# Kernel tuning notes

Measured on AMD Instinct MI355X. Metric: run time of the kernel, lower is better.

## Reference

```python
import jax, jax.numpy as jnp
import numpy as np
import math

EMBED_DIM = 768
NUM_HEADS = 12
MLP_HIDDEN = int(EMBED_DIM * 2.0)
LN_EPS = 1e-6


def _complex_linear(r, i, wr, wi, br, bi):
    # (r + i*j) @ (wr + wi*j)^T + (br + bi*j)
    out_r = r @ wr.T - i @ wi.T + br
    out_i = r @ wi.T + i @ wr.T + bi
    return out_r, out_i


def _complex_layernorm(r, i, gamma, beta):
    # magnitude-based LN over feature dim; gamma/beta: [F, 2]
    mag = jnp.sqrt(r * r + i * i + LN_EPS)           # [..., F]
    mean = mag.mean(axis=-1, keepdims=True)
    var = ((mag - mean) ** 2).mean(axis=-1, keepdims=True)  # unbiased=False
    norm_mag = (mag - mean) / jnp.sqrt(var + LN_EPS)
    scale = norm_mag / (mag + LN_EPS)
    r_n = r * scale
    i_n = i * scale
    return gamma[..., 0] * r_n + beta[..., 0], gamma[..., 1] * i_n + beta[..., 1]


def setup_inputs() -> dict:
    key = jax.random.key(0)
    ks = jax.random.split(key, 12)
    B, N, E, H = 2, 2048, EMBED_DIM, MLP_HIDDEN
    std_qkv = math.sqrt(2.0 / (E + 3 * E))
    std_proj = math.sqrt(2.0 / (E + E))
    std_fc1 = math.sqrt(2.0 / (E + H))
    std_fc2 = math.sqrt(2.0 / (H + E))
    inp = {
        "x": jax.random.normal(ks[0], (B, N, 2 * E), dtype=jnp.float32),
        "norm1_gamma": 1.0 + 0.1 * jax.random.normal(ks[1], (E, 2), dtype=jnp.float32),
        "norm1_beta": 0.1 * jax.random.normal(ks[2], (E, 2), dtype=jnp.float32),
        "qkv_wr": std_qkv * jax.random.normal(ks[3], (3 * E, E), dtype=jnp.float32),
        "qkv_wi": std_qkv * jax.random.normal(ks[4], (3 * E, E), dtype=jnp.float32),
        "qkv_br": jnp.zeros((3 * E,), dtype=jnp.float32),
        "qkv_bi": jnp.zeros((3 * E,), dtype=jnp.float32),
        "proj_wr": std_proj * jax.random.normal(ks[5], (E, E), dtype=jnp.float32),
        "proj_wi": std_proj * jax.random.normal(ks[6], (E, E), dtype=jnp.float32),
        "proj_br": jnp.zeros((E,), dtype=jnp.float32),
        "proj_bi": jnp.zeros((E,), dtype=jnp.float32),
        "norm2_gamma": 1.0 + 0.1 * jax.random.normal(ks[7], (E, 2), dtype=jnp.float32),
        "norm2_beta": 0.1 * jax.random.normal(ks[8], (E, 2), dtype=jnp.float32),
        "fc1_wr": std_fc1 * jax.random.normal(ks[9], (H, E), dtype=jnp.float32),
        "fc1_wi": std_fc1 * jax.random.normal(ks[10], (H, E), dtype=jnp.float32),
        "fc1_br": jnp.zeros((H,), dtype=jnp.float32),
        "fc1_bi": jnp.zeros((H,), dtype=jnp.float32),
        "fc2_wr": std_fc2 * jax.random.normal(ks[11], (E, H), dtype=jnp.float32),
        "fc2_wi": std_fc2 * jax.random.normal(jax.random.fold_in(key, 99), (E, H), dtype=jnp.float32),
        "fc2_br": jnp.zeros((E,), dtype=jnp.float32),
        "fc2_bi": jnp.zeros((E,), dtype=jnp.float32),
    }
    return inp


def reference(x, norm1_gamma, norm1_beta, qkv_wr, qkv_wi, qkv_br, qkv_bi,
              proj_wr, proj_wi, proj_br, proj_bi, norm2_gamma, norm2_beta,
              fc1_wr, fc1_wi, fc1_br, fc1_bi, fc2_wr, fc2_wi, fc2_br, fc2_bi):
    B, N, _ = x.shape
    E, nH = EMBED_DIM, NUM_HEADS
    hd = E // nH
    xc = x.reshape(B, N, E, 2)
    xr, xi = xc[..., 0], xc[..., 1]

    # --- attention branch ---
    nr, ni = _complex_layernorm(xr, xi, norm1_gamma, norm1_beta)
    qkv_r, qkv_i = _complex_linear(nr, ni, qkv_wr, qkv_wi, qkv_br, qkv_bi)  # [B,N,3E]
    # split to [3, B, nH, N, hd]
    def split_heads(t):
        return t.reshape(B, N, 3, nH, hd).transpose(2, 0, 3, 1, 4)
    qkv_r = split_heads(qkv_r)
    qkv_i = split_heads(qkv_i)
    qr, kr, vr = qkv_r[0], qkv_r[1], qkv_r[2]
    qi, ki, vi = qkv_i[0], qkv_i[1], qkv_i[2]

    # complex attention scores: q * conj-free formulation per source
    attn_real = jnp.einsum('bhqd,bhkd->bhqk', qr, kr) + jnp.einsum('bhqd,bhkd->bhqk', qi, ki)
    attn_imag = jnp.einsum('bhqd,bhkd->bhqk', qr, ki) - jnp.einsum('bhqd,bhkd->bhqk', qi, kr)
    attn_mag = jnp.sqrt(attn_real ** 2 + attn_imag ** 2 + 1e-8) / math.sqrt(hd)
    attn_w = jax.nn.softmax(attn_mag, axis=-1)
    out_r = jnp.einsum('bhqk,bhkd->bhqd', attn_w, vr)
    out_i = jnp.einsum('bhqk,bhkd->bhqd', attn_w, vi)
    # [B,nH,N,hd] -> [B,N,E]
    out_r = out_r.transpose(0, 2, 1, 3).reshape(B, N, E)
    out_i = out_i.transpose(0, 2, 1, 3).reshape(B, N, E)
    pr, pi = _complex_linear(out_r, out_i, proj_wr, proj_wi, proj_br, proj_bi)
    xr = xr + pr
    xi = xi + pi

    # --- MLP branch ---
    nr2, ni2 = _complex_layernorm(xr, xi, norm2_gamma, norm2_beta)
    h_r, h_i = _complex_linear(nr2, ni2, fc1_wr, fc1_wi, fc1_br, fc1_bi)
    h_r = jax.nn.gelu(h_r, approximate=False)
    h_i = jax.nn.gelu(h_i, approximate=False)
    m_r, m_i = _complex_linear(h_r, h_i, fc2_wr, fc2_wi, fc2_br, fc2_bi)
    xr = xr + m_r
    xi = xi + m_i

    return jnp.stack([xr, xi], axis=-1).reshape(B, N, 2 * E)
```

## Files before the change

### kernel.cpp

```cpp
#include <hip/hip_runtime.h>
#include <cmath>

typedef __bf16 bf16;
typedef __bf16 bf16x8 __attribute__((ext_vector_type(8)));
typedef __bf16 bf16x4 __attribute__((ext_vector_type(4)));
typedef float  f32x4  __attribute__((ext_vector_type(4)));
typedef unsigned int u32x4 __attribute__((ext_vector_type(4)));

#define MFMA16(a, b, c) __builtin_amdgcn_mfma_f32_16x16x32_bf16((a), (b), (c), 0, 0, 0)
#define LOG2E 1.44269504088896f

static __device__ __forceinline__ void gl_lds16(const void* g, void* l) {
    __builtin_amdgcn_global_load_lds((const __attribute__((address_space(1))) void*)g,
                                     (__attribute__((address_space(3))) void*)l, 16, 0, 0);
}

static __device__ __forceinline__ bf16x8 bneg8(bf16x8 x) {
    u32x4 u = __builtin_bit_cast(u32x4, x);
    u = u ^ 0x80008000u;
    return __builtin_bit_cast(bf16x8, u);
}

static __device__ __forceinline__ f32x4 zero4() {
    return f32x4{0.0f, 0.0f, 0.0f, 0.0f};
}

__global__ void fill_kernel(float* p, float v, int n) {
    for (int i = blockIdx.x * blockDim.x + threadIdx.x; i < n; i += gridDim.x * blockDim.x)
        p[i] = v;
}

struct Cvt8 {
    const float* s[8];
    bf16* d[8];
    int boff[9];
    int cvtBlocks;
};
__global__ __launch_bounds__(256) void prep_kernel(
    Cvt8 c, const float* __restrict__ x,
    const float* __restrict__ gamma, const float* __restrict__ beta,
    bf16* __restrict__ nr, bf16* __restrict__ ni) {
    const int t = threadIdx.x;
    if ((int)blockIdx.x < c.cvtBlocks) {
        int blk = blockIdx.x;
        int seg = 0;
#pragma unroll
        for (int k = 0; k < 7; ++k)
            if (blk >= c.boff[k + 1]) seg = k + 1;
        const int local = blk - c.boff[seg];
        const int i = local * 1024 + t * 4;
        const float4 v = *(const float4*)(c.s[seg] + i);
        bf16x4 o;
        o[0] = (bf16)v.x; o[1] = (bf16)v.y; o[2] = (bf16)v.z; o[3] = (bf16)v.w;
        *(bf16x4*)(c.d[seg] + i) = o;
        return;
    }
    __shared__ float red[4];
    const size_t base = (size_t)(blockIdx.x - c.cvtBlocks) * 768;
    float r[3], im[3], mg[3];
#pragma unroll
    for (int j = 0; j < 3; ++j) {
        const int f = t + j * 256;
        const float2 v = ((const float2*)x)[base + f];
        r[j] = v.x;
        im[j] = v.y;
        mg[j] = __builtin_amdgcn_sqrtf(r[j] * r[j] + im[j] * im[j] + 1e-6f);
    }
    float s = mg[0] + mg[1] + mg[2];
#pragma unroll
    for (int m = 32; m >= 1; m >>= 1) s += __shfl_xor(s, m);
    if ((t & 63) == 0) red[t >> 6] = s;
    __syncthreads();
    const float mean = (red[0] + red[1] + red[2] + red[3]) * (1.0f / 768.0f);
    __syncthreads();
    float v2 = 0.0f;
#pragma unroll
    for (int j = 0; j < 3; ++j) {
        const float d = mg[j] - mean;
        v2 += d * d;
    }
#pragma unroll
    for (int m = 32; m >= 1; m >>= 1) v2 += __shfl_xor(v2, m);
    if ((t & 63) == 0) red[t >> 6] = v2;
    __syncthreads();
    const float var = (red[0] + red[1] + red[2] + red[3]) * (1.0f / 768.0f);
    const float rstd = rsqrtf(var + 1e-6f);
#pragma unroll
    for (int j = 0; j < 3; ++j) {
        const int f = t + j * 256;
        const float sc = (mg[j] - mean) * rstd / (mg[j] + 1e-6f);
        nr[base + f] = (bf16)(gamma[2 * f] * (r[j] * sc) + beta[2 * f]);
        ni[base + f] = (bf16)(gamma[2 * f + 1] * (im[j] * sc) + beta[2 * f + 1]);
    }
}

__global__ __launch_bounds__(256) void cln2_kernel(
    const bf16* __restrict__ xa, const bf16* __restrict__ xb,
    const float* __restrict__ gamma, const float* __restrict__ beta,
    bf16* __restrict__ nr, bf16* __restrict__ ni) {
    __shared__ float red[4];
    const int t = threadIdx.x;
    const size_t base = (size_t)blockIdx.x * 768;

    float r[3], im[3], mg[3];
#pragma unroll
    for (int j = 0; j < 3; ++j) {
        const int f = t + j * 256;
        r[j] = (float)xa[base + f];
        im[j] = (float)xb[base + f];
        mg[j] = __builtin_amdgcn_sqrtf(r[j] * r[j] + im[j] * im[j] + 1e-6f);
    }
    float s = mg[0] + mg[1] + mg[2];
#pragma unroll
    for (int m = 32; m >= 1; m >>= 1) s += __shfl_xor(s, m);
    if ((t & 63) == 0) red[t >> 6] = s;
    __syncthreads();
    const float mean = (red[0] + red[1] + red[2] + red[3]) * (1.0f / 768.0f);
    __syncthreads();

    float v2 = 0.0f;
#pragma unroll
    for (int j = 0; j < 3; ++j) {
        const float d = mg[j] - mean;
        v2 += d * d;
    }
#pragma unroll
    for (int m = 32; m >= 1; m >>= 1) v2 += __shfl_xor(v2, m);
    if ((t & 63) == 0) red[t >> 6] = v2;
    __syncthreads();
    const float var = (red[0] + red[1] + red[2] + red[3]) * (1.0f / 768.0f);
    const float rstd = rsqrtf(var + 1e-6f);

#pragma unroll
    for (int j = 0; j < 3; ++j) {
        const int f = t + j * 256;
        const float sc = (mg[j] - mean) * rstd / (mg[j] + 1e-6f);
        nr[base + f] = (bf16)(gamma[2 * f] * (r[j] * sc) + beta[2 * f]);
        ni[base + f] = (bf16)(gamma[2 * f + 1] * (im[j] * sc) + beta[2 * f + 1]);
    }
}

template <int BM, int BN, int MODE, int OCC, bool SWZC>
__global__ __launch_bounds__(256, OCC) void cgemm_kernel(
    const bf16* __restrict__ Ar, const bf16* __restrict__ Ai,
    const bf16* __restrict__ Wr, const bf16* __restrict__ Wi,
    const float* __restrict__ br, const float* __restrict__ bi,
    const void* __restrict__ resr, const void* __restrict__ resi,
    float* __restrict__ outFr, float* __restrict__ outFi,
    bf16* __restrict__ outBr, bf16* __restrict__ outBi,
    int N, int K) {
    constexpr int MR = BM / 32;
    constexpr int NR = BN / 32;
    constexpr int ASEG = BM / 8;
    constexpr int NSEG = (BM + BN) / 8;
    constexpr int SPW = NSEG / 4;

    __shared__ __align__(16) bf16 sA[2][BM][64];
    __shared__ __align__(16) bf16 sB[2][BN][64];

    const int tid = threadIdx.x;
    const int wave = tid >> 6, lane = tid & 63;
    const int lg = lane >> 4, lr = lane & 15;

    const int bid = blockIdx.y * gridDim.x + blockIdx.x;
    const int xcd = bid & 7;
    const int i = bid >> 3;
    int rowb, colb;
    if (SWZC) {
        const int cpx = gridDim.y >> 3;
        colb = xcd * cpx + (i % cpx);
        rowb = i / cpx;
    } else {
        const int rpx = gridDim.x >> 3;
        rowb = xcd * rpx + (i % rpx);
        colb = i / rpx;
    }
    const int row0 = rowb * BM, col0 = colb * BN;

    const int wm = (wave >> 1) * (BM / 2), wn = (wave & 1) * (BN / 2);

    const int srow = lane >> 3;
    const int schunk = (lane & 7) ^ srow;
    const int spl = schunk >> 2;
    const int sc8 = (schunk & 3) * 8;

    auto issue = [&](int buf, int kt) {
#pragma unroll
        for (int s = 0; s < SPW; ++s) {
            const int id = wave * SPW + s;
            if (id < ASEG) {
                const int row = id * 8 + srow;
                gl_lds16((spl ? Ai : Ar) + (size_t)(row0 + row) * K + kt + sc8,
                         &sA[buf][id * 8][0]);
            } else {
                const int row = (id - ASEG) * 8 + srow;
                gl_lds16((spl ? Wi : Wr) + (size_t)(col0 + row) * K + kt + sc8,
                         &sB[buf][(id - ASEG) * 8][0]);
            }
        }
    };

    f32x4 accr[MR][NR], acci[MR][NR];
#pragma unroll
    for (int a = 0; a < MR; ++a)
#pragma unroll
        for (int b2 = 0; b2 < NR; ++b2) {
            accr[a][b2] = zero4();
            acci[a][b2] = zero4();
        }

    issue(0, 0);

    const int KT = K / 32;
    for (int kt = 0; kt < KT; ++kt) {
        const int buf = kt & 1;
        if (kt + 1 < KT) {
            issue(buf ^ 1, (kt + 1) * 32);
            __builtin_amdgcn_sched_barrier(0);
            if constexpr (SPW == 8)
                asm volatile("s_waitcnt vmcnt(8)" ::: "memory");
            else if constexpr (SPW == 6)
                asm volatile("s_waitcnt vmcnt(6)" ::: "memory");
            else
                asm volatile("s_waitcnt vmcnt(0)" ::: "memory");
        } else {
            asm volatile("s_waitcnt vmcnt(0)" ::: "memory");
        }
        __builtin_amdgcn_sched_barrier(0);
        __builtin_amdgcn_s_barrier();
        __builtin_amdgcn_sched_barrier(0);

        bf16x8 ar[MR], ai[MR], an[MR];
#pragma unroll
        for (int mt = 0; mt < MR; ++mt) {
            const int rr = wm + mt * 16 + lr;
            const int slr = lg ^ (rr & 7);
            const int sli = (4 + lg) ^ (rr & 7);
            ar[mt] = *(const bf16x8*)(&sA[buf][rr][slr * 8]);
            ai[mt] = *(const bf16x8*)(&sA[buf][rr][sli * 8]);
            an[mt] = bneg8(ai[mt]);
        }
        __builtin_amdgcn_s_setprio(1);
#pragma unroll
        for (int nt = 0; nt < NR; ++nt) {
            const int rr = wn + nt * 16 + lr;
            const int slr = lg ^ (rr & 7);
            const int sli = (4 + lg) ^ (rr & 7);
            const bf16x8 br8 = *(const bf16x8*)(&sB[buf][rr][slr * 8]);
            const bf16x8 bi8 = *(const bf16x8*)(&sB[buf][rr][sli * 8]);
#pragma unroll
            for (int mt = 0; mt < MR; ++mt) {
                accr[mt][nt] = MFMA16(ar[mt], br8, accr[mt][nt]);
                accr[mt][nt] = MFMA16(an[mt], bi8, accr[mt][nt]);
                acci[mt][nt] = MFMA16(ar[mt], bi8, acci[mt][nt]);
                acci[mt][nt] = MFMA16(ai[mt], br8, acci[mt][nt]);
            }
        }
        __builtin_amdgcn_s_setprio(0);

        if (kt + 1 < KT) {
            __builtin_amdgcn_sched_barrier(0);
            __builtin_amdgcn_s_barrier();
            __builtin_amdgcn_sched_barrier(0);
        }
    }

#pragma unroll
    for (int nt = 0; nt < NR; ++nt) {
        const int col = col0 + wn + nt * 16 + lr;
        const float bre = br[col], bie = bi[col];
#pragma unroll
        for (int mt = 0; mt < MR; ++mt) {
#pragma unroll
            for (int j = 0; j < 4; ++j) {
                const int row = row0 + wm + mt * 16 + lg * 4 + j;
                float vr = accr[mt][nt][j] + bre;
                float vi = acci[mt][nt][j] + bie;
                const size_t o = (size_t)row * N + col;
                if (MODE == 1) {
                    const float2 rv = ((const float2*)resr)[(size_t)row * 768 + col];
                    outBr[o] = (bf16)(rv.x + vr);
                    outBi[o] = (bf16)(rv.y + vi);
                } else if (MODE == 2) {
                    const float t2r = fmaf(vr * vr, 0.044715f, 1.0f);
                    const float er = __builtin_amdgcn_exp2f(vr * t2r * 2.3022082f);
                    vr = vr - vr * __builtin_amdgcn_rcpf(er + 1.0f);
                    const float t2i = fmaf(vi * vi, 0.044715f, 1.0f);
                    const float ei = __builtin_amdgcn_exp2f(vi * t2i * 2.3022082f);
                    vi = vi - vi * __builtin_amdgcn_rcpf(ei + 1.0f);
                    outBr[o] = (bf16)vr;
                    outBi[o] = (bf16)vi;
                } else {
                    const size_t ro = (size_t)row * 768 + col;
                    outFr[(size_t)row * 1536 + 2 * col] =
                        (float)((const bf16*)resr)[ro] + vr;
                    outFr[(size_t)row * 1536 + 2 * col + 1] =
                        (float)((const bf16*)resi)[ro] + vi;
                }
            }
        }
    }
}

__global__ __launch_bounds__(256, 3) void qkvt_kernel(
    const bf16* __restrict__ nr, const bf16* __restrict__ ni,
    const bf16* __restrict__ wqr, const bf16* __restrict__ wqi,
    const float* __restrict__ qbr, const float* __restrict__ qbi,
    bf16* __restrict__ qkr, bf16* __restrict__ qki,
    bf16* __restrict__ vtr, bf16* __restrict__ vti) {
    constexpr int BM = 64, BN = 128, K = 768;
    constexpr int MR = 2, NR = 4, ASEG = 8, SPW = 6;
    constexpr int HHE = 1536 * 768;

    __shared__ __align__(16) bf16 sA[2][BM][64];
    __shared__ __align__(16) bf16 sB[2][BN][64];

    const int tid = threadIdx.x;
    const int wave = tid >> 6, lane = tid & 63;
    const int lg = lane >> 4, lr = lane & 15;

    const bool isQK = (int)blockIdx.x < 768;
    const bf16 *Ar, *Ai, *Wr, *Wi;
    bf16 *outR, *outI;
    int N, row0, col0;
    if (isQK) {
        const int bid = blockIdx.x;
        const int xcd = bid & 7, i = bid >> 3;
        row0 = (xcd * 8 + (i & 7)) * BM;
        col0 = (i >> 3) * BN;
        Ar = nr; Ai = ni; Wr = wqr; Wi = wqi;
        outR = qkr; outI = qki; N = 1536;
    } else {
        const int bid = blockIdx.x - 768;
        const int xcd = bid & 7, i = bid >> 3;
        col0 = (xcd * 4 + (i & 3)) * BN;
        row0 = (i >> 2) * BM;
        Ar = wqr + HHE; Ai = wqi + HHE; Wr = nr; Wi = ni;
        outR = vtr; outI = vti; N = 4096;
    }

    const int wm = (wave >> 1) * (BM / 2), wn = (wave & 1) * (BN / 2);
    const int srow = lane >> 3;
    const int schunk = (lane & 7) ^ srow;
    const int spl = schunk >> 2;
    const int sc8 = (schunk & 3) * 8;

    auto issue = [&](int buf, int kt) {
#pragma unroll
        for (int s = 0; s < SPW; ++s) {
            const int id = wave * SPW + s;
            if (id < ASEG) {
                const int row = id * 8 + srow;
                gl_lds16((spl ? Ai : Ar) + (size_t)(row0 + row) * K + kt + sc8,
                         &sA[buf][id * 8][0]);
            } else {
                const int row = (id - ASEG) * 8 + srow;
                gl_lds16((spl ? Wi : Wr) + (size_t)(col0 + row) * K + kt + sc8,
                         &sB[buf][(id - ASEG) * 8][0]);
            }
        }
    };

    f32x4 accr[MR][NR], acci[MR][NR];
#pragma unroll
    for (int a = 0; a < MR; ++a)
#pragma unroll
        for (int b2 = 0; b2 < NR; ++b2) {
            accr[a][b2] = zero4();
            acci[a][b2] = zero4();
        }

    issue(0, 0);

    const int KT = K / 32;
    for (int kt = 0; kt < KT; ++kt) {
        const int buf = kt & 1;
        if (kt + 1 < KT) {
            issue(buf ^ 1, (kt + 1) * 32);
            __builtin_amdgcn_sched_barrier(0);
            asm volatile("s_waitcnt vmcnt(6)" ::: "memory");
        } else {
            asm volatile("s_waitcnt vmcnt(0)" ::: "memory");
        }
        __builtin_amdgcn_sched_barrier(0);
        __builtin_amdgcn_s_barrier();
        __builtin_amdgcn_sched_barrier(0);

        bf16x8 ar[MR], ai[MR], an[MR];
#pragma unroll
        for (int mt = 0; mt < MR; ++mt) {
            const int rr = wm + mt * 16 + lr;
            const int slr = lg ^ (rr & 7);
            const int sli = (4 + lg) ^ (rr & 7);
            ar[mt] = *(const bf16x8*)(&sA[buf][rr][slr * 8]);
            ai[mt] = *(const bf16x8*)(&sA[buf][rr][sli * 8]);
            an[mt] = bneg8(ai[mt]);
        }
        __builtin_amdgcn_s_setprio(1);
#pragma unroll
        for (int nt = 0; nt < NR; ++nt) {
            const int rr = wn + nt * 16 + lr;
            const int slr = lg ^ (rr & 7);
            const int sli = (4 + lg) ^ (rr & 7);
            const bf16x8 br8 = *(const bf16x8*)(&sB[buf][rr][slr * 8]);
            const bf16x8 bi8 = *(const bf16x8*)(&sB[buf][rr][sli * 8]);
#pragma unroll
            for (int mt = 0; mt < MR; ++mt) {
                accr[mt][nt] = MFMA16(ar[mt], br8, accr[mt][nt]);
                accr[mt][nt] = MFMA16(an[mt], bi8, accr[mt][nt]);
                acci[mt][nt] = MFMA16(ar[mt], bi8, acci[mt][nt]);
                acci[mt][nt] = MFMA16(ai[mt], br8, acci[mt][nt]);
            }
        }
        __builtin_amdgcn_s_setprio(0);

        if (kt + 1 < KT) {
            __builtin_amdgcn_sched_barrier(0);
            __builtin_amdgcn_s_barrier();
            __builtin_amdgcn_sched_barrier(0);
        }
    }

#pragma unroll
    for (int nt = 0; nt < NR; ++nt) {
        const int col = col0 + wn + nt * 16 + lr;
        const float bre = isQK ? qbr[col] : 0.0f;
        const float bie = isQK ? qbi[col] : 0.0f;
#pragma unroll
        for (int mt = 0; mt < MR; ++mt) {
#pragma unroll
            for (int j = 0; j < 4; ++j) {
                const int row = row0 + wm + mt * 16 + lg * 4 + j;
                float vr = accr[mt][nt][j];
                float vi = acci[mt][nt][j];
                if (isQK) {
                    vr += bre;
                    vi += bie;
                } else {
                    vr += qbr[1536 + row];
                    vi += qbi[1536 + row];
                }
                const size_t o = (size_t)row * N + col;
                outR[o] = (bf16)vr;
                outI[o] = (bf16)vi;
            }
        }
    }
}

__global__ __launch_bounds__(256, 3) void cattn_kernel(
    const bf16* __restrict__ qkr, const bf16* __restrict__ qki,
    const bf16* __restrict__ vtr, const bf16* __restrict__ vti,
    bf16* __restrict__ aor, bf16* __restrict__ aoi) {
    __shared__ __align__(16) bf16 sK[3][2][32][64];
    __shared__ __align__(16) bf16 sV[3][64][64];
    __shared__ __align__(16) bf16 sP[4][16][40];

    const int tid = threadIdx.x;
    const int w = tid >> 6, lane = tid & 63;
    const int lg = lane >> 4, lr = lane & 15;

    const int bid = blockIdx.x;
    const int xcd = bid & 7;
    const int i = bid >> 3;
    const int grp = xcd * 3 + (i >> 5);
    const int qb = i & 31;
    const int h = grp % 12, b = grp / 12;
    const int ld = 1536;

    const int s_krow = lane >> 3;
    const int s_kch8 = ((lane & 7) ^ s_krow) * 8;
    const int s_vlog = (lane & 7) ^ s_krow;
    const int s_vpl = s_vlog >> 2;
    const int s_vk8 = (s_vlog & 3) * 8;

    const bf16* kbase0 = qkr + (size_t)b * 2048 * ld + 768 + h * 64;
    const bf16* kbase1 = qki + (size_t)b * 2048 * ld + 768 + h * 64;
    const bf16* vbase = (s_vpl ? vti : vtr) + (size_t)(h * 64) * 4096 + b * 2048;

    const bf16* kp0 = kbase0 + (size_t)(w * 8 + s_krow) * ld + s_kch8;
    const bf16* kp1 = kbase1 + (size_t)(w * 8 + s_krow) * ld + s_kch8;
    const bf16* vp0 = vbase + (size_t)(w * 8 + s_krow) * 4096 + s_vk8;
    const bf16* vp1 = vbase + (size_t)((4 + w) * 8 + s_krow) * 4096 + s_vk8;

    auto stage = [&](int slot) {
        gl_lds16(kp0, &sK[slot][0][w * 8][0]);
        gl_lds16(kp1, &sK[slot][1][w * 8][0]);
        gl_lds16(vp0, &sV[slot][w * 8][0]);
        gl_lds16(vp1, &sV[slot][(4 + w) * 8][0]);
        kp0 += 32 * ld;
        kp1 += 32 * ld;
        vp0 += 32;
        vp1 += 32;
    };

    stage(0);

    const size_t qoff = (size_t)(b * 2048 + qb * 64 + w * 16 + lr) * ld + h * 64;
    bf16x8 aqr[2], aqi[2], aqin[2];
#pragma unroll
    for (int ks = 0; ks < 2; ++ks) {
        aqr[ks] = *(const bf16x8*)(qkr + qoff + ks * 32 + lg * 8);
        aqi[ks] = *(const bf16x8*)(qki + qoff + ks * 32 + lg * 8);
        aqin[ks] = bneg8(aqi[ks]);
    }

    f32x4 our[4], oui[4];
#pragma unroll
    for (int d = 0; d < 4; ++d) {
        our[d] = zero4();
        oui[d] = zero4();
    }
    const float C1 = 0.125f * LOG2E;
    float mrun = -1e30f;
    float lrun_p = 0.0f;
    float thr2 = -1.0f;
    float mC2 = 0.0f;

    int cur = 0;
    const int slr = lg ^ (lr & 7);
    const int sli = (4 + lg) ^ (lr & 7);

    for (int kt = 0; kt < 64; ++kt) {
        int nxt = cur + 1;
        if (nxt == 3) nxt = 0;
        if (kt < 63) {
            stage(nxt);
            __builtin_amdgcn_sched_barrier(0);
            asm volatile("s_waitcnt vmcnt(4)" ::: "memory");
        } else {
            asm volatile("s_waitcnt vmcnt(0)" ::: "memory");
        }
        __builtin_amdgcn_sched_barrier(0);
        __builtin_amdgcn_s_barrier();
        __builtin_amdgcn_sched_barrier(0);

        f32x4 str[2], sti[2];
        str[0] = zero4(); str[1] = zero4();
        sti[0] = zero4(); sti[1] = zero4();
        __builtin_amdgcn_s_setprio(1);
#pragma unroll
        for (int t = 0; t < 2; ++t) {
#pragma unroll
            for (int ks = 0; ks < 2; ++ks) {
                const int ch = ((ks << 2) | lg) ^ (lr & 7);
                const bf16x8 kr8 = *(const bf16x8*)(&sK[cur][0][t * 16 + lr][ch * 8]);
                const bf16x8 ki8 = *(const bf16x8*)(&sK[cur][1][t * 16 + lr][ch * 8]);
                str[t] = MFMA16(kr8, aqr[ks], str[t]);
                str[t] = MFMA16(ki8, aqi[ks], str[t]);
                sti[t] = MFMA16(ki8, aqr[ks], sti[t]);
                sti[t] = MFMA16(kr8, aqin[ks], sti[t]);
            }
        }
        __builtin_amdgcn_s_setprio(0);

        float v[8];
        float vmax = 0.0f;
#pragma unroll
        for (int t = 0; t < 2; ++t)
#pragma unroll
            for (int j = 0; j < 4; ++j) {
                const float sr = str[t][j], si = sti[t][j];
                const float vv = fmaf(sr, sr, fmaf(si, si, 1e-8f));
                v[t * 4 + j] = vv;
                vmax = fmaxf(vmax, vv);
            }

        if (!__all(vmax <= thr2)) {
            vmax = fmaxf(vmax, __shfl_xor(vmax, 16));
            vmax = fmaxf(vmax, __shfl_xor(vmax, 32));
            const float tm = __builtin_amdgcn_sqrtf(vmax) * 0.125f;
            const float mnew = fmaxf(mrun, tm);
            const float corr = __builtin_amdgcn_exp2f((mrun - mnew) * LOG2E);
            float cj[4];
#pragma unroll
            for (int j = 0; j < 4; ++j) cj[j] = __shfl(corr, lg * 4 + j);
#pragma unroll
            for (int d = 0; d < 4; ++d)
#pragma unroll
                for (int j = 0; j < 4; ++j) {
                    our[d][j] *= cj[j];
                    oui[d][j] *= cj[j];
                }
            lrun_p *= corr;
            mrun = mnew;
            const float m8 = mrun + 8.0f;
            thr2 = 64.0f * m8 * m8;
            mC2 = -mrun * LOG2E;
        }

        float p[8];
        float ls = 0.0f;
#pragma unroll
        for (int i2 = 0; i2 < 8; ++i2) {
            p[i2] = __builtin_amdgcn_exp2f(
                fmaf(__builtin_amdgcn_sqrtf(v[i2]), C1, mC2));
            ls += p[i2];
        }
        lrun_p += ls;

#pragma unroll
        for (int t = 0; t < 2; ++t) {
            bf16x4 pk;
#pragma unroll
            for (int j = 0; j < 4; ++j) pk[j] = (bf16)p[t * 4 + j];
            *(bf16x4*)(&sP[w][lr][t * 16 + lg * 4]) = pk;
        }
        const bf16x8 pf = *(const bf16x8*)(&sP[w][lr][lg * 8]);

        __builtin_amdgcn_s_setprio(1);
#pragma unroll
        for (int d = 0; d < 4; ++d) {
            const bf16x8 vr8 = *(const bf16x8*)(&sV[cur][d * 16 + lr][slr * 8]);
            const bf16x8 vi8 = *(const bf16x8*)(&sV[cur][d * 16 + lr][sli * 8]);
            our[d] = MFMA16(pf, vr8, our[d]);
            oui[d] = MFMA16(pf, vi8, oui[d]);
        }
        __builtin_amdgcn_s_setprio(0);

        cur = nxt;
    }

    float lsum = lrun_p;
    lsum += __shfl_xor(lsum, 16);
    lsum += __shfl_xor(lsum, 32);

    float linv[4];
#pragma unroll
    for (int j = 0; j < 4; ++j) {
        const float lj = __shfl(lsum, lg * 4 + j);
        linv[j] = __builtin_amdgcn_rcpf(lj);
    }
#pragma unroll
    for (int d = 0; d < 4; ++d)
#pragma unroll
        for (int j = 0; j < 4; ++j) {
            const int row = b * 2048 + qb * 64 + w * 16 + lg * 4 + j;
            const int col = h * 64 + d * 16 + lr;
            aor[(size_t)row * 768 + col] = (bf16)(our[d][j] * linv[j]);
            aoi[(size_t)row * 768 + col] = (bf16)(oui[d][j] * linv[j]);
        }
}

extern "C" void kernel_launch(void* const* d_in, const int* in_sizes, int n_in,
                              void* d_out, int out_size, void* d_ws, size_t ws_size,
                              hipStream_t stream) {
    const float* x      = (const float*)d_in[0];
    const float* n1g    = (const float*)d_in[1];
    const float* n1b    = (const float*)d_in[2];
    const float* qkvwr  = (const float*)d_in[3];
    const float* qkvwi  = (const float*)d_in[4];
    const float* qkvbr  = (const float*)d_in[5];
    const float* qkvbi  = (const float*)d_in[6];
    const float* projwr = (const float*)d_in[7];
    const float* projwi = (const float*)d_in[8];
    const float* projbr = (const float*)d_in[9];
    const float* projbi = (const float*)d_in[10];
    const float* n2g    = (const float*)d_in[11];
    const float* n2b    = (const float*)d_in[12];
    const float* fc1wr  = (const float*)d_in[13];
    const float* fc1wi  = (const float*)d_in[14];
    const float* fc1br  = (const float*)d_in[15];
    const float* fc1bi  = (const float*)d_in[16];
    const float* fc2wr  = (const float*)d_in[17];
    const float* fc2wi  = (const float*)d_in[18];
    const float* fc2br  = (const float*)d_in[19];
    const float* fc2bi  = (const float*)d_in[20];

    const int M = 4096, E = 768, E3 = 2304, HH = 1536;

    char* base = (char*)d_ws;
    size_t off = 0;
    auto alloc = [&](size_t bytes) -> void* {
        void* p = base + off;
        off += (bytes + 255) & ~(size_t)255;
        return p;
    };
    bf16* xr2  = (bf16*)alloc((size_t)M * E * 2);
    bf16* xi2  = (bf16*)alloc((size_t)M * E * 2);
    bf16* nr   = (bf16*)alloc((size_t)M * E * 2);
    bf16* ni   = (bf16*)alloc((size_t)M * E * 2);
    bf16* wqr  = (bf16*)alloc((size_t)E3 * E * 2);
    bf16* wqi  = (bf16*)alloc((size_t)E3 * E * 2);
    bf16* wpr  = (bf16*)alloc((size_t)E * E * 2);
    bf16* wpi  = (bf16*)alloc((size_t)E * E * 2);
    bf16* w1r  = (bf16*)alloc((size_t)HH * E * 2);
    bf16* w1i  = (bf16*)alloc((size_t)HH * E * 2);
    bf16* w2r  = (bf16*)alloc((size_t)E * HH * 2);
    bf16* w2i  = (bf16*)alloc((size_t)E * HH * 2);
    bf16* qkr  = (bf16*)alloc((size_t)M * HH * 2);
    bf16* qki  = (bf16*)alloc((size_t)M * HH * 2);
    bf16* vtr  = (bf16*)alloc((size_t)E * M * 2);
    bf16* vti  = (bf16*)alloc((size_t)E * M * 2);
    bf16* aor  = (bf16*)alloc((size_t)M * E * 2);
    bf16* aoi  = (bf16*)alloc((size_t)M * E * 2);
    bf16* hr   = (bf16*)alloc((size_t)M * HH * 2);
    bf16* hi   = (bf16*)alloc((size_t)M * HH * 2);

    if (off > ws_size) {
        fill_kernel<<<1024, 256, 0, stream>>>((float*)d_out, 1.0e9f, out_size);
        return;
    }

    Cvt8 c;
    c.s[0] = qkvwr; c.d[0] = wqr;
    c.s[1] = qkvwi; c.d[1] = wqi;
    c.s[2] = projwr; c.d[2] = wpr;
    c.s[3] = projwi; c.d[3] = wpi;
    c.s[4] = fc1wr; c.d[4] = w1r;
    c.s[5] = fc1wi; c.d[5] = w1i;
    c.s[6] = fc2wr; c.d[6] = w2r;
    c.s[7] = fc2wi; c.d[7] = w2i;
    const int nseg[8] = {E3 * E, E3 * E, E * E, E * E, HH * E, HH * E, E * HH, E * HH};
    int cum = 0;
    for (int k = 0; k < 8; ++k) {
        c.boff[k] = cum;
        cum += nseg[k] / 1024;
    }
    c.boff[8] = cum;
    c.cvtBlocks = cum;
    prep_kernel<<<cum + M, 256, 0, stream>>>(c, x, n1g, n1b, nr, ni);

    qkvt_kernel<<<1152, 256, 0, stream>>>(nr, ni, wqr, wqi, qkvbr, qkvbi,
                                          qkr, qki, vtr, vti);
    cattn_kernel<<<768, 256, 0, stream>>>(qkr, qki, vtr, vti, aor, aoi);
    cgemm_kernel<128, 64, 1, 3, false><<<dim3(32, 12), 256, 0, stream>>>(
        aor, aoi, wpr, wpi, projbr, projbi, x, nullptr, nullptr, nullptr,
        xr2, xi2, E, E);
    cln2_kernel<<<M, 256, 0, stream>>>(xr2, xi2, n2g, n2b, nr, ni);
    cgemm_kernel<64, 128, 2, 3, false><<<dim3(64, 12), 256, 0, stream>>>(
        nr, ni, w1r, w1i, fc1br, fc1bi, nullptr, nullptr, nullptr, nullptr,
        hr, hi, HH, E);
    cgemm_kernel<128, 64, 3, 3, false><<<dim3(32, 12), 256, 0, stream>>>(
        hr, hi, w2r, w2i, fc2br, fc2bi, xr2, xi2, (float*)d_out, nullptr,
        nullptr, nullptr, E, HH);
}
```

Measured before the change: 335.3 us.

## Software-pipeline attention PV matmul one tile behind QK with split K/V buffers

The attention loop now defers the P·V MFMAs for tile kt-1 into iteration kt, issuing them right after the QK^T MFMAs. The softmax exp/sqrt work can then overlap with matrix-core work instead of serializing. K staging drops to a double buffer while V keeps a triple buffer. An extra workgroup barrier per iteration is added to protect the buffer reuse. The deferred PV must also handle the online-max rescale correctly, since the accumulator may be rescaled before the previous tile's P is applied.

```diff
diff --git a/kernel.cpp b/kernel.cpp
--- a/kernel.cpp
+++ b/kernel.cpp
@@ -452,7 +452,7 @@
     const bf16* __restrict__ qkr, const bf16* __restrict__ qki,
     const bf16* __restrict__ vtr, const bf16* __restrict__ vti,
     bf16* __restrict__ aor, bf16* __restrict__ aoi) {
-    __shared__ __align__(16) bf16 sK[3][2][32][64];
+    __shared__ __align__(16) bf16 sK[2][2][32][64];
     __shared__ __align__(16) bf16 sV[3][64][64];
     __shared__ __align__(16) bf16 sP[4][16][40];
 
@@ -483,18 +483,18 @@
     const bf16* vp0 = vbase + (size_t)(w * 8 + s_krow) * 4096 + s_vk8;
     const bf16* vp1 = vbase + (size_t)((4 + w) * 8 + s_krow) * 4096 + s_vk8;
 
-    auto stage = [&](int slot) {
-        gl_lds16(kp0, &sK[slot][0][w * 8][0]);
-        gl_lds16(kp1, &sK[slot][1][w * 8][0]);
-        gl_lds16(vp0, &sV[slot][w * 8][0]);
-        gl_lds16(vp1, &sV[slot][(4 + w) * 8][0]);
+    auto stage = [&](int kb, int vs) {
+        gl_lds16(kp0, &sK[kb][0][w * 8][0]);
+        gl_lds16(kp1, &sK[kb][1][w * 8][0]);
+        gl_lds16(vp0, &sV[vs][w * 8][0]);
+        gl_lds16(vp1, &sV[vs][(4 + w) * 8][0]);
         kp0 += 32 * ld;
         kp1 += 32 * ld;
         vp0 += 32;
         vp1 += 32;
     };
 
-    stage(0);
+    stage(0, 0);
 
     const size_t qoff = (size_t)(b * 2048 + qb * 64 + w * 16 + lr) * ld + h * 64;
     bf16x8 aqr[2], aqi[2], aqin[2];
@@ -517,15 +517,17 @@
     float thr2 = -1.0f;
     float mC2 = 0.0f;
 
-    int cur = 0;
+    bf16x8 pfPrev = __builtin_bit_cast(bf16x8, u32x4{0u, 0u, 0u, 0u});
+    int vcur = 0, vlast = 0;
     const int slr = lg ^ (lr & 7);
     const int sli = (4 + lg) ^ (lr & 7);
 
     for (int kt = 0; kt < 64; ++kt) {
-        int nxt = cur + 1;
-        if (nxt == 3) nxt = 0;
+        const int kcur = kt & 1;
+        int vnext = vcur + 1;
+        if (vnext == 3) vnext = 0;
         if (kt < 63) {
-            stage(nxt);
+            stage(kcur ^ 1, vnext);
             __builtin_amdgcn_sched_barrier(0);
             asm volatile("s_waitcnt vmcnt(4)" ::: "memory");
         } else {
@@ -544,12 +546,21 @@
 #pragma unroll
             for (int ks = 0; ks < 2; ++ks) {
                 const int ch = ((ks << 2) | lg) ^ (lr & 7);
-                const bf16x8 kr8 = *(const bf16x8*)(&sK[cur][0][t * 16 + lr][ch * 8]);
-                const bf16x8 ki8 = *(const bf16x8*)(&sK[cur][1][t * 16 + lr][ch * 8]);
+                const bf16x8 kr8 = *(const bf16x8*)(&sK[kcur][0][t * 16 + lr][ch * 8]);
+                const bf16x8 ki8 = *(const bf16x8*)(&sK[kcur][1][t * 16 + lr][ch * 8]);
                 str[t] = MFMA16(kr8, aqr[ks], str[t]);
                 str[t] = MFMA16(ki8, aqi[ks], str[t]);
                 sti[t] = MFMA16(ki8, aqr[ks], sti[t]);
                 sti[t] = MFMA16(kr8, aqin[ks], sti[t]);
+            }
+        }
+        if (kt > 0) {
+#pragma unroll
+            for (int d = 0; d < 4; ++d) {
+                const bf16x8 vr8 = *(const bf16x8*)(&sV[vlast][d * 16 + lr][slr * 8]);
+                const bf16x8 vi8 = *(const bf16x8*)(&sV[vlast][d * 16 + lr][sli * 8]);
+                our[d] = MFMA16(pfPrev, vr8, our[d]);
+                oui[d] = MFMA16(pfPrev, vi8, oui[d]);
             }
         }
         __builtin_amdgcn_s_setprio(0);
@@ -606,19 +617,22 @@
             for (int j = 0; j < 4; ++j) pk[j] = (bf16)p[t * 4 + j];
             *(bf16x4*)(&sP[w][lr][t * 16 + lg * 4]) = pk;
         }
-        const bf16x8 pf = *(const bf16x8*)(&sP[w][lr][lg * 8]);
-
-        __builtin_amdgcn_s_setprio(1);
-#pragma unroll
-        for (int d = 0; d < 4; ++d) {
-            const bf16x8 vr8 = *(const bf16x8*)(&sV[cur][d * 16 + lr][slr * 8]);
-            const bf16x8 vi8 = *(const bf16x8*)(&sV[cur][d * 16 + lr][sli * 8]);
-            our[d] = MFMA16(pf, vr8, our[d]);
-            oui[d] = MFMA16(pf, vi8, oui[d]);
-        }
-        __builtin_amdgcn_s_setprio(0);
-
-        cur = nxt;
+        pfPrev = *(const bf16x8*)(&sP[w][lr][lg * 8]);
+
+        vlast = vcur;
+        vcur = vnext;
+
+        __builtin_amdgcn_sched_barrier(0);
+        __builtin_amdgcn_s_barrier();
+        __builtin_amdgcn_sched_barrier(0);
+    }
+
+#pragma unroll
+    for (int d = 0; d < 4; ++d) {
+        const bf16x8 vr8 = *(const bf16x8*)(&sV[vlast][d * 16 + lr][slr * 8]);
+        const bf16x8 vi8 = *(const bf16x8*)(&sV[vlast][d * 16 + lr][sli * 8]);
+        our[d] = MFMA16(pfPrev, vr8, our[d]);
+        oui[d] = MFMA16(pfPrev, vi8, oui[d]);
     }
 
     float lsum = lrun_p;
```

Measured after the change: 306.8 us. 1.09x faster.
